# Kernel tuning notes

Measured on AMD Instinct MI355X. Metric: run time of the kernel, lower is better.

The kernel has to match this reference:

```python
import jax, jax.numpy as jnp
import numpy as np

D = 512
B = 8
N = 4096  # h = w = 64 grid


def _rmsnorm(x, eps=1e-6):
    # SimpleRMSNorm (no learned scale)
    return x * jax.lax.rsqrt(jnp.mean(jnp.square(x), axis=-1, keepdims=True) + eps)


def setup_inputs() -> dict:
    key = jax.random.key(0)
    ks = jax.random.split(key, 8)
    s = 1.0 / np.sqrt(D)
    return {
        "x": jax.random.normal(ks[0], (B, N, D), jnp.float32),
        "lower_bound": jax.random.uniform(ks[1], (1,), jnp.float32),
        "W_in": jax.random.normal(ks[2], (D, D), jnp.float32) * s,
        "b_in": jnp.zeros((D,), jnp.float32),
        "W_f": jax.random.normal(ks[3], (D, D), jnp.float32) * s,
        "b_f": jnp.zeros((D,), jnp.float32),
        "theta": jax.random.normal(ks[4], (D,), jnp.float32),
        "W_g": jax.random.normal(ks[5], (D, D), jnp.float32) * s,
        "b_g": jnp.zeros((D,), jnp.float32),
        "W_out": jax.random.normal(ks[6], (D, D), jnp.float32) * s,
        "b_out": jnp.zeros((D,), jnp.float32),
    }


def _gated_scan(decay, u, axis, reverse):
    # linear recurrence h_t = decay_t * h_{t-1} + u_t via associative scan
    def comb(e1, e2):
        a1, x1 = e1
        a2, x2 = e2
        return a1 * a2, a2 * x1 + x2
    _, y = jax.lax.associative_scan(comb, (decay, u), axis=axis, reverse=reverse)
    return y


def reference(x, lower_bound, W_in, b_in, W_f, b_f, theta, W_g, b_g, W_out, b_out):
    b, n, d = x.shape
    h = int(np.sqrt(n))
    w = n // h
    # b n d -> n b d -> h w b d
    xg = jnp.transpose(x, (1, 0, 2)).reshape(h, w, b, d)
    u = jax.nn.silu(xg @ W_in + b_in)              # candidate input
    f = jax.nn.sigmoid(xg @ W_f + b_f)             # forget gate
    lam = lower_bound + (1.0 - lower_bound) * f    # lower-bounded decay magnitude
    # complex decay lam * exp(i theta); complex input (1 - lam) * u
    decay = (lam * jnp.cos(theta) + 1j * (lam * jnp.sin(theta))).astype(jnp.complex64)
    inp = ((1.0 - lam) * u).astype(jnp.complex64)
    # bidirectional 2D scan: forward/backward over both grid axes (non-causal)
    hidden = jnp.zeros_like(u)
    for axis in (0, 1):
        for rev in (False, True):
            hidden = hidden + _gated_scan(decay, inp, axis, rev).real
    g = jax.nn.sigmoid(xg @ W_g + b_g)             # output gate
    y = (g * _rmsnorm(hidden)) @ W_out + b_out
    # h w b d -> n b d -> b n d
    return jnp.transpose(y.reshape(n, b, d), (1, 0, 2))
```

## Files before the change

### kernel.cpp

```cpp
#include <hip/hip_runtime.h>
#include <math.h>

#define DD 512
#define HG 64
#define M_ROWS 32768
#define ELEMS ((size_t)M_ROWS * DD)
#define LOG2E 1.44269504088896340736f

typedef __attribute__((ext_vector_type(8))) _Float16 f16x8;
typedef __attribute__((ext_vector_type(2))) _Float16 f16x2;
typedef __attribute__((ext_vector_type(4))) float f32x4;

__device__ __forceinline__ float fexp2_(float x) { return __builtin_amdgcn_exp2f(x); }
__device__ __forceinline__ float frcp_(float x)  { return __builtin_amdgcn_rcpf(x); }
__device__ __forceinline__ float fsig_(float v)  { return frcp_(1.0f + fexp2_(-v * LOG2E)); }

__global__ __launch_bounds__(256) void prep(
    const float* __restrict__ x, _Float16* __restrict__ x16,
    const float* __restrict__ W0, const float* __restrict__ W1,
    const float* __restrict__ W2, const float* __restrict__ W3,
    _Float16* __restrict__ WT)
{
    __shared__ float tile[64][65];
    if (blockIdx.x < 8192) {
        const size_t i = ((size_t)blockIdx.x * 256 + threadIdx.x) * 8;
        const float4 a = *(const float4*)&x[i];
        const float4 b = *(const float4*)&x[i + 4];
        f16x8 h;
        h[0] = (_Float16)a.x; h[1] = (_Float16)a.y;
        h[2] = (_Float16)a.z; h[3] = (_Float16)a.w;
        h[4] = (_Float16)b.x; h[5] = (_Float16)b.y;
        h[6] = (_Float16)b.z; h[7] = (_Float16)b.w;
        *(f16x8*)&x16[i] = h;
        return;
    }
    const int wb = blockIdx.x - 8192;
    const int z = wb >> 6;
    const int rem = wb & 63;
    const int n0 = (rem & 7) * 64, k0 = (rem >> 3) * 64;
    const float* W = (z == 0) ? W0 : (z == 1) ? W1 : (z == 2) ? W2 : W3;
    _Float16* dst = WT + (size_t)z * DD * DD;
    const int t = threadIdx.x;
    const int tr = t >> 6, tc = t & 63;
#pragma unroll
    for (int p = 0; p < 16; ++p)
        tile[p * 4 + tr][tc] = W[(size_t)(k0 + p * 4 + tr) * DD + n0 + tc];
    __syncthreads();
#pragma unroll
    for (int p = 0; p < 16; ++p) {
        const int nn = p * 4 + tr;
        dst[(size_t)(n0 + nn) * DD + k0 + tc] = (_Float16)tile[tc][nn];
    }
}

template <int MODE>
__global__ __launch_bounds__(256) void gemm_f16(
    const _Float16* __restrict__ A, const _Float16* __restrict__ WT,
    const float* __restrict__ b0, const float* __restrict__ b1,
    const float* __restrict__ b2, const float* __restrict__ lb_ptr,
    void* __restrict__ o0, void* __restrict__ o1, void* __restrict__ o2)
{
    __shared__ __align__(16) _Float16 As[2][128][32];
    __shared__ __align__(16) _Float16 Bs[2][128][32];

    const int NB = (MODE == 0) ? 12 : 4;
    const int lin = blockIdx.x;
    const int xcd = lin & 7;
    const int n_idx = (lin >> 3) % NB;
    const int mq = lin / (8 * NB);
    const int m0 = (xcd + 8 * mq) * 128;
    const int n0 = n_idx * 128;

    const int tid  = threadIdx.x;
    const int wave = tid >> 6;
    const int lane = tid & 63;
    const int wm = wave >> 1, wn = wave & 1;
    const int lrow = lane & 15;
    const int lk   = lane >> 4;

    const int srow  = lane >> 2;
    const int skoff = ((lane & 3) ^ ((lane >> 3) & 3)) * 8;
    const int ksw   = (lk ^ ((lrow >> 1) & 3)) * 8;

    f32x4 acc[4][4];
#pragma unroll
    for (int i = 0; i < 4; ++i)
#pragma unroll
        for (int j = 0; j < 4; ++j) acc[i][j] = (f32x4)(0.f);

    for (int k0 = 0; k0 < DD; k0 += 64) {
#pragma unroll
        for (int h = 0; h < 2; ++h) {
#pragma unroll
            for (int i = 0; i < 2; ++i) {
                const int row = wave * 32 + i * 16;
                const _Float16* bsrc =
                    WT + (size_t)(n0 + row + srow) * DD + k0 + h * 32 + skoff;
                __builtin_amdgcn_global_load_lds(
                    (const __attribute__((address_space(1))) void*)bsrc,
                    (__attribute__((address_space(3))) void*)&Bs[h][row][0], 16, 0, 0);
                const _Float16* asrc =
                    A + (size_t)(m0 + row + srow) * DD + k0 + h * 32 + skoff;
                __builtin_amdgcn_global_load_lds(
                    (const __attribute__((address_space(1))) void*)asrc,
                    (__attribute__((address_space(3))) void*)&As[h][row][0], 16, 0, 0);
            }
        }
        __syncthreads();
#pragma unroll
        for (int h = 0; h < 2; ++h) {
            f16x8 afr[4], bfr[4];
#pragma unroll
            for (int t = 0; t < 4; ++t) {
                afr[t] = *(const f16x8*)&As[h][wm * 64 + t * 16 + lrow][ksw];
                bfr[t] = *(const f16x8*)&Bs[h][wn * 64 + t * 16 + lrow][ksw];
            }
#pragma unroll
            for (int mt = 0; mt < 4; ++mt)
#pragma unroll
                for (int nt = 0; nt < 4; ++nt)
                    acc[mt][nt] = __builtin_amdgcn_mfma_f32_16x16x32_f16(
                        afr[mt], bfr[nt], acc[mt][nt], 0, 0, 0);
        }
        __syncthreads();
    }

    if (MODE == 0) {
        const int seg = n_idx >> 2;
        const float lbv = lb_ptr[0];
        const float* bias = (seg == 0) ? b0 : (seg == 1) ? b1 : b2;
        _Float16* outp = (seg == 0) ? (_Float16*)o0
                       : (seg == 1) ? (_Float16*)o1 : (_Float16*)o2;
        const int cb = (n_idx & 3) * 128 + wn * 64;
#pragma unroll
        for (int mt = 0; mt < 4; ++mt) {
#pragma unroll
            for (int nt = 0; nt < 4; ++nt) {
                const int col = cb + nt * 16 + lrow;
                const float bcol = bias[col];
#pragma unroll
                for (int r = 0; r < 4; ++r) {
                    const int row = m0 + wm * 64 + mt * 16 + lk * 4 + r;
                    const float v = acc[mt][nt][r] + bcol;
                    float res;
                    if (seg == 0)      res = (1.0f - lbv) * frcp_(1.0f + fexp2_(v * LOG2E));
                    else if (seg == 1) res = v * fsig_(v);
                    else               res = fsig_(v);
                    outp[(size_t)row * DD + col] = (_Float16)res;
                }
            }
        }
    } else {
        float* outp = (float*)o0;
#pragma unroll
        for (int mt = 0; mt < 4; ++mt) {
#pragma unroll
            for (int nt = 0; nt < 4; ++nt) {
                const int col = n0 + wn * 64 + nt * 16 + lrow;
                const float bcol = b0[col];
#pragma unroll
                for (int r = 0; r < 4; ++r) {
                    const int row = m0 + wm * 64 + mt * 16 + lk * 4 + r;
                    outp[(size_t)row * DD + col] = acc[mt][nt][r] + bcol;
                }
            }
        }
    }
}

#define CH 4
#define CL 16

#define STEP(K, YR0, YI0, YR1, YI1) {                                      \
    const float dm0_ = (float)dmr[K][0], dm1_ = (float)dmr[K][1];          \
    const float lm0_ = 1.0f - dm0_, lm1_ = 1.0f - dm1_;                    \
    float nr_ = fmaf(lm0_, c0 * (YR0) - s0 * (YI0), dm0_ * (float)ur[K][0]); \
    YI0 = lm0_ * (c0 * (YI0) + s0 * (YR0)); YR0 = nr_;                     \
    nr_ = fmaf(lm1_, c1 * (YR1) - s1 * (YI1), dm1_ * (float)ur[K][1]);     \
    YI1 = lm1_ * (c1 * (YI1) + s1 * (YR1)); YR1 = nr_; }

__global__ __launch_bounds__(256, 4) void scan2(
    const _Float16* __restrict__ dm, const _Float16* __restrict__ u,
    const float* __restrict__ theta,
    _Float16* __restrict__ ha, _Float16* __restrict__ hb)
{
    __shared__ float ex[CH][64][13];

    const int blk  = blockIdx.x & 2047;
    const bool is_i = blockIdx.x >= 2048;
    const int tid   = threadIdx.x;
    const int chunk = tid >> 6;
    const int dpl   = tid & 63;
    const int dpg   = blk & 3;
    const int line  = blk >> 2;
    const int d0    = (dpg * 64 + dpl) * 2;

    size_t base, stride;
    _Float16* hout;
    if (!is_i) {
        base = (size_t)line * (HG * DD) + d0; stride = DD; hout = ha;
    } else {
        const int bb = line >> 6, j = line & 63;
        base = (size_t)bb * (HG * HG * DD) + (size_t)j * DD + d0;
        stride = (size_t)HG * DD; hout = hb;
    }
    const size_t cbase = base + (size_t)(chunk * CL) * stride;

    float s0, c0, s1, c1;
    sincosf(theta[d0], &s0, &c0);
    sincosf(theta[d0 + 1], &s1, &c1);

    f16x2 dmr[CL], ur[CL];
#pragma unroll
    for (int k = 0; k < CL; ++k) {
        dmr[k] = *(const f16x2*)&dm[cbase + (size_t)k * stride];
        ur[k]  = *(const f16x2*)&u [cbase + (size_t)k * stride];
    }

    float fr0 = 0.f, fi0 = 0.f, fr1 = 0.f, fi1 = 0.f;
    float P0 = 1.f, P1 = 1.f;
#pragma unroll
    for (int k = 0; k < CL; ++k) {
        const float dm0_ = (float)dmr[k][0], dm1_ = (float)dmr[k][1];
        const float lm0_ = 1.0f - dm0_, lm1_ = 1.0f - dm1_;
        P0 *= lm0_; P1 *= lm1_;
        float nr_ = fmaf(lm0_, c0 * fr0 - s0 * fi0, dm0_ * (float)ur[k][0]);
        fi0 = lm0_ * (c0 * fi0 + s0 * fr0); fr0 = nr_;
        nr_ = fmaf(lm1_, c1 * fr1 - s1 * fi1, dm1_ * (float)ur[k][1]);
        fi1 = lm1_ * (c1 * fi1 + s1 * fr1); fr1 = nr_;
    }
    float br0 = 0.f, bi0 = 0.f, br1 = 0.f, bi1 = 0.f;
#pragma unroll
    for (int k = CL - 1; k >= 0; --k) STEP(k, br0, bi0, br1, bi1);

    float rc0 = c0, rs0 = s0, rc1 = c1, rs1 = s1;
#pragma unroll
    for (int q = 0; q < 4; ++q) {
        float t0 = rc0 * rc0 - rs0 * rs0; rs0 = 2.f * rc0 * rs0; rc0 = t0;
        float t1 = rc1 * rc1 - rs1 * rs1; rs1 = 2.f * rc1 * rs1; rc1 = t1;
    }

    {
        float* e = ex[chunk][dpl];
        e[0]  = P0 * rc0; e[1]  = P0 * rs0;
        e[2]  = fr0;      e[3]  = fi0;
        e[4]  = br0;      e[5]  = bi0;
        e[6]  = P1 * rc1; e[7]  = P1 * rs1;
        e[8]  = fr1;      e[9]  = fi1;
        e[10] = br1;      e[11] = bi1;
    }
    __syncthreads();

    float cfr0 = 0.f, cfi0 = 0.f, cfr1 = 0.f, cfi1 = 0.f;
    for (int cc = 0; cc < chunk; ++cc) {
        const float* e = ex[cc][dpl];
        float nr = e[2] + e[0] * cfr0 - e[1] * cfi0;
        cfi0     = e[3] + e[0] * cfi0 + e[1] * cfr0;
        cfr0 = nr;
        nr       = e[8] + e[6] * cfr1 - e[7] * cfi1;
        cfi1     = e[9] + e[6] * cfi1 + e[7] * cfr1;
        cfr1 = nr;
    }
    float cbr0 = 0.f, cbi0 = 0.f, cbr1 = 0.f, cbi1 = 0.f;
    for (int cc = CH - 1; cc > chunk; --cc) {
        const float* e = ex[cc][dpl];
        float nr = e[4] + e[0] * cbr0 - e[1] * cbi0;
        cbi0     = e[5] + e[0] * cbi0 + e[1] * cbr0;
        cbr0 = nr;
        nr       = e[10] + e[6] * cbr1 - e[7] * cbi1;
        cbi1     = e[11] + e[6] * cbi1 + e[7] * cbr1;
        cbr1 = nr;
    }

    float yr0 = cfr0, yi0 = cfi0, yr1 = cfr1, yi1 = cfi1;
    f16x2 fres[CL];
#pragma unroll
    for (int k = 0; k < CL; ++k) {
        STEP(k, yr0, yi0, yr1, yi1);
        f16x2 p; p[0] = (_Float16)yr0; p[1] = (_Float16)yr1;
        fres[k] = p;
    }
    yr0 = cbr0; yi0 = cbi0; yr1 = cbr1; yi1 = cbi1;
#pragma unroll
    for (int k = CL - 1; k >= 0; --k) {
        STEP(k, yr0, yi0, yr1, yi1);
        f16x2 o;
        o[0] = (_Float16)((float)fres[k][0] + yr0);
        o[1] = (_Float16)((float)fres[k][1] + yr1);
        *(f16x2*)&hout[cbase + (size_t)k * stride] = o;
    }
}
#undef STEP

__global__ __launch_bounds__(256) void gate_rmsnorm(
    const _Float16* __restrict__ ha, const _Float16* __restrict__ hb,
    const _Float16* __restrict__ g, _Float16* __restrict__ v)
{
    const int row = blockIdx.x;
    const int t = threadIdx.x;
    const size_t b0 = (size_t)row * DD + t * 2;
    const f16x2 a = *(const f16x2*)&ha[b0];
    const f16x2 b = *(const f16x2*)&hb[b0];
    const float h0 = (float)a[0] + (float)b[0];
    const float h1 = (float)a[1] + (float)b[1];
    float ss = h0 * h0 + h1 * h1;
#pragma unroll
    for (int off = 32; off > 0; off >>= 1) ss += __shfl_down(ss, off, 64);
    __shared__ float wsum[4];
    __shared__ float rms_s;
    if ((t & 63) == 0) wsum[t >> 6] = ss;
    __syncthreads();
    if (t == 0) {
        const float tot = wsum[0] + wsum[1] + wsum[2] + wsum[3];
        rms_s = rsqrtf(tot * (1.0f / (float)DD) + 1e-6f);
    }
    __syncthreads();
    const float rms = rms_s;
    const f16x2 gg = *(const f16x2*)&g[b0];
    f16x2 o;
    o[0] = (_Float16)((float)gg[0] * h0 * rms);
    o[1] = (_Float16)((float)gg[1] * h1 * rms);
    *(f16x2*)&v[b0] = o;
}

extern "C" void kernel_launch(void* const* d_in, const int* in_sizes, int n_in,
                              void* d_out, int out_size, void* d_ws, size_t ws_size,
                              hipStream_t stream)
{
    const float* x     = (const float*)d_in[0];
    const float* lb    = (const float*)d_in[1];
    const float* W_in  = (const float*)d_in[2];
    const float* b_in  = (const float*)d_in[3];
    const float* W_f   = (const float*)d_in[4];
    const float* b_f   = (const float*)d_in[5];
    const float* theta = (const float*)d_in[6];
    const float* W_g   = (const float*)d_in[7];
    const float* b_g   = (const float*)d_in[8];
    const float* W_out = (const float*)d_in[9];
    const float* b_out = (const float*)d_in[10];

    float* out = (float*)d_out;
    char* wsb  = (char*)d_ws;

    _Float16* dm_v = (_Float16*)wsb;
    _Float16* u_b  = (_Float16*)(wsb + ELEMS * 2);
    _Float16* g_b  = (_Float16*)(wsb + ELEMS * 4);
    _Float16* WT   = (_Float16*)(wsb + ELEMS * 6);
    const size_t WSEG = (size_t)DD * DD;

    _Float16* ha  = (_Float16*)d_out;
    _Float16* x16 = (_Float16*)((char*)d_out + ELEMS * 2);
    _Float16* hb  = x16;

    prep<<<8448, 256, 0, stream>>>(x, x16, W_f, W_in, W_g, W_out, WT);

    gemm_f16<0><<<3072, 256, 0, stream>>>(x16, WT, b_f, b_in, b_g, lb,
                                          dm_v, u_b, g_b);

    scan2<<<4096, 256, 0, stream>>>(dm_v, u_b, theta, ha, hb);

    gate_rmsnorm<<<M_ROWS, 256, 0, stream>>>(ha, hb, g_b, dm_v);

    gemm_f16<1><<<1024, 256, 0, stream>>>(dm_v, WT + 3 * WSEG, b_out, nullptr,
                                          nullptr, nullptr, out, nullptr, nullptr);
}
```

Before: 292.8 us.

## Triple-buffer GEMM K-loop with async LDS loads and single barrier per step

Replaces the double-sync, load-then-compute K loop of the f16 MFMA GEMM with a 3-stage ring buffer in shared memory. Global-to-LDS loads are issued two 32-wide K slices ahead, and a partial vmcnt wait plus one barrier per step lets loads overlap the MFMA work. It also raises wave priority around the MFMA block with s_setprio. The cost is more LDS per block, which can lower occupancy, and correctness depends on the hand-written vmcnt counts.

Result: no change. 295.9 us (+1.0%).

```diff
diff --git a/kernel.cpp b/kernel.cpp
--- a/kernel.cpp
+++ b/kernel.cpp
@@ -60,8 +60,8 @@
     const float* __restrict__ b2, const float* __restrict__ lb_ptr,
     void* __restrict__ o0, void* __restrict__ o1, void* __restrict__ o2)
 {
-    __shared__ __align__(16) _Float16 As[2][128][32];
-    __shared__ __align__(16) _Float16 Bs[2][128][32];
+    __shared__ __align__(16) _Float16 As[3][128][32];
+    __shared__ __align__(16) _Float16 Bs[3][128][32];
 
     const int NB = (MODE == 0) ? 12 : 4;
     const int lin = blockIdx.x;
@@ -82,48 +82,64 @@
     const int skoff = ((lane & 3) ^ ((lane >> 3) & 3)) * 8;
     const int ksw   = (lk ^ ((lrow >> 1) & 3)) * 8;
 
+    const _Float16* a_base = A  + (size_t)(m0 + srow) * DD + skoff;
+    const _Float16* b_base = WT + (size_t)(n0 + srow) * DD + skoff;
+
     f32x4 acc[4][4];
 #pragma unroll
     for (int i = 0; i < 4; ++i)
 #pragma unroll
         for (int j = 0; j < 4; ++j) acc[i][j] = (f32x4)(0.f);
 
-    for (int k0 = 0; k0 < DD; k0 += 64) {
-#pragma unroll
-        for (int h = 0; h < 2; ++h) {
-#pragma unroll
-            for (int i = 0; i < 2; ++i) {
-                const int row = wave * 32 + i * 16;
-                const _Float16* bsrc =
-                    WT + (size_t)(n0 + row + srow) * DD + k0 + h * 32 + skoff;
-                __builtin_amdgcn_global_load_lds(
-                    (const __attribute__((address_space(1))) void*)bsrc,
-                    (__attribute__((address_space(3))) void*)&Bs[h][row][0], 16, 0, 0);
-                const _Float16* asrc =
-                    A + (size_t)(m0 + row + srow) * DD + k0 + h * 32 + skoff;
-                __builtin_amdgcn_global_load_lds(
-                    (const __attribute__((address_space(1))) void*)asrc,
-                    (__attribute__((address_space(3))) void*)&As[h][row][0], 16, 0, 0);
-            }
+#define STAGE(S, KK) do {                                                     \
+    _Pragma("unroll")                                                         \
+    for (int i_ = 0; i_ < 2; ++i_) {                                          \
+        const int row_ = wave * 32 + i_ * 16;                                 \
+        __builtin_amdgcn_global_load_lds(                                     \
+            (const __attribute__((address_space(1))) void*)                   \
+                (b_base + (size_t)row_ * DD + (KK)),                          \
+            (__attribute__((address_space(3))) void*)&Bs[S][row_][0], 16, 0, 0); \
+        __builtin_amdgcn_global_load_lds(                                     \
+            (const __attribute__((address_space(1))) void*)                   \
+                (a_base + (size_t)row_ * DD + (KK)),                          \
+            (__attribute__((address_space(3))) void*)&As[S][row_][0], 16, 0, 0); \
+    } } while (0)
+
+#define COMPUTE(S) do {                                                       \
+    f16x8 afr[4], bfr[4];                                                     \
+    _Pragma("unroll")                                                         \
+    for (int q_ = 0; q_ < 4; ++q_) {                                          \
+        afr[q_] = *(const f16x8*)&As[S][wm * 64 + q_ * 16 + lrow][ksw];       \
+        bfr[q_] = *(const f16x8*)&Bs[S][wn * 64 + q_ * 16 + lrow][ksw];       \
+    }                                                                         \
+    __builtin_amdgcn_s_setprio(1);                                            \
+    _Pragma("unroll")                                                         \
+    for (int mt_ = 0; mt_ < 4; ++mt_)                                         \
+        _Pragma("unroll")                                                     \
+        for (int nt_ = 0; nt_ < 4; ++nt_)                                     \
+            acc[mt_][nt_] = __builtin_amdgcn_mfma_f32_16x16x32_f16(           \
+                afr[mt_], bfr[nt_], acc[mt_][nt_], 0, 0, 0);                  \
+    __builtin_amdgcn_s_setprio(0);                                            \
+    } while (0)
+
+    STAGE(0, 0);
+    STAGE(1, 32);
+    int rs = 0, ws = 2;
+    for (int t = 0; t < 15; ++t) {
+        asm volatile("s_waitcnt vmcnt(4)" ::: "memory");
+        __builtin_amdgcn_s_barrier();
+        if (t < 14) {
+            STAGE(ws, (t + 2) * 32);
+            ws = (ws == 2) ? 0 : ws + 1;
         }
-        __syncthreads();
-#pragma unroll
-        for (int h = 0; h < 2; ++h) {
-            f16x8 afr[4], bfr[4];
-#pragma unroll
-            for (int t = 0; t < 4; ++t) {
-                afr[t] = *(const f16x8*)&As[h][wm * 64 + t * 16 + lrow][ksw];
-                bfr[t] = *(const f16x8*)&Bs[h][wn * 64 + t * 16 + lrow][ksw];
-            }
-#pragma unroll
-            for (int mt = 0; mt < 4; ++mt)
-#pragma unroll
-                for (int nt = 0; nt < 4; ++nt)
-                    acc[mt][nt] = __builtin_amdgcn_mfma_f32_16x16x32_f16(
-                        afr[mt], bfr[nt], acc[mt][nt], 0, 0, 0);
-        }
-        __syncthreads();
-    }
+        COMPUTE(rs);
+        rs = (rs == 2) ? 0 : rs + 1;
+    }
+    asm volatile("s_waitcnt vmcnt(0)" ::: "memory");
+    __builtin_amdgcn_s_barrier();
+    COMPUTE(rs);
+#undef STAGE
+#undef COMPUTE
 
     if (MODE == 0) {
         const int seg = n_idx >> 2;
```

## Rewrite GEMMs as 256x256-tile 8-wave kernel with interleaved async LDS prefetch

Applied to the files above, without the earlier changes.

Replaces the 128x128 double-buffered GEMM with a 256x256 tile, 512-thread kernel that runs over 64-wide K-steps. It interleaves global_load_lds prefetches of the next stages with MFMA quarters, using explicit vmcnt waits, barriers and setprio. It also applies an XOR swizzle on 128-byte LDS rows. The aim is higher arithmetic intensity and overlap of loads with MFMA work, at the cost of 128 KB of LDS per block, many more accumulator registers, and fewer blocks (768 and 256) that may underfill the GPU's CUs.

Result: faster. 283.0 us (-3.4%).

```diff
diff --git a/kernel.cpp b/kernel.cpp
--- a/kernel.cpp
+++ b/kernel.cpp
@@ -54,115 +54,188 @@
 }
 
 template <int MODE>
-__global__ __launch_bounds__(256) void gemm_f16(
+__global__ __launch_bounds__(512, 2) void gemm8p(
     const _Float16* __restrict__ A, const _Float16* __restrict__ WT,
     const float* __restrict__ b0, const float* __restrict__ b1,
     const float* __restrict__ b2, const float* __restrict__ lb_ptr,
     void* __restrict__ o0, void* __restrict__ o1, void* __restrict__ o2)
 {
-    __shared__ __align__(16) _Float16 As[2][128][32];
-    __shared__ __align__(16) _Float16 Bs[2][128][32];
-
-    const int NB = (MODE == 0) ? 12 : 4;
+    __shared__ __align__(16) _Float16 As[2][256][64];
+    __shared__ __align__(16) _Float16 Bs[2][256][64];
+
+    const int NB = (MODE == 0) ? 6 : 2;
     const int lin = blockIdx.x;
     const int xcd = lin & 7;
-    const int n_idx = (lin >> 3) % NB;
-    const int mq = lin / (8 * NB);
-    const int m0 = (xcd + 8 * mq) * 128;
-    const int n0 = n_idx * 128;
+    const int qq  = lin >> 3;
+    const int n_idx = qq % NB;
+    const int mq  = qq / NB;
+    const int m0 = (xcd + 8 * mq) * 256;
+    const int n0 = n_idx * 256;
 
     const int tid  = threadIdx.x;
-    const int wave = tid >> 6;
+    const int wv   = tid >> 6;
     const int lane = tid & 63;
-    const int wm = wave >> 1, wn = wave & 1;
+    const int wm = wv >> 2, wn = wv & 3;
     const int lrow = lane & 15;
     const int lk   = lane >> 4;
 
-    const int srow  = lane >> 2;
-    const int skoff = ((lane & 3) ^ ((lane >> 3) & 3)) * 8;
-    const int ksw   = (lk ^ ((lrow >> 1) & 3)) * 8;
-
-    f32x4 acc[4][4];
-#pragma unroll
-    for (int i = 0; i < 4; ++i)
+    const int srow8 = wv * 8 + (lane >> 3);
+    const int sswz  = ((lane & 7) ^ (lane >> 3)) * 8;
+
+    const _Float16* Ag = A  + (size_t)m0 * DD;
+    const _Float16* Bg = WT + (size_t)n0 * DD;
+
+    f32x4 acc[8][4];
+#pragma unroll
+    for (int i = 0; i < 8; ++i)
 #pragma unroll
         for (int j = 0; j < 4; ++j) acc[i][j] = (f32x4)(0.f);
 
-    for (int k0 = 0; k0 < DD; k0 += 64) {
-#pragma unroll
-        for (int h = 0; h < 2; ++h) {
-#pragma unroll
-            for (int i = 0; i < 2; ++i) {
-                const int row = wave * 32 + i * 16;
-                const _Float16* bsrc =
-                    WT + (size_t)(n0 + row + srow) * DD + k0 + h * 32 + skoff;
-                __builtin_amdgcn_global_load_lds(
-                    (const __attribute__((address_space(1))) void*)bsrc,
-                    (__attribute__((address_space(3))) void*)&Bs[h][row][0], 16, 0, 0);
-                const _Float16* asrc =
-                    A + (size_t)(m0 + row + srow) * DD + k0 + h * 32 + skoff;
-                __builtin_amdgcn_global_load_lds(
-                    (const __attribute__((address_space(1))) void*)asrc,
-                    (__attribute__((address_space(3))) void*)&As[h][row][0], 16, 0, 0);
-            }
-        }
-        __syncthreads();
-#pragma unroll
-        for (int h = 0; h < 2; ++h) {
-            f16x8 afr[4], bfr[4];
-#pragma unroll
-            for (int t = 0; t < 4; ++t) {
-                afr[t] = *(const f16x8*)&As[h][wm * 64 + t * 16 + lrow][ksw];
-                bfr[t] = *(const f16x8*)&Bs[h][wn * 64 + t * 16 + lrow][ksw];
-            }
-#pragma unroll
-            for (int mt = 0; mt < 4; ++mt)
-#pragma unroll
-                for (int nt = 0; nt < 4; ++nt)
-                    acc[mt][nt] = __builtin_amdgcn_mfma_f32_16x16x32_f16(
-                        afr[mt], bfr[nt], acc[mt][nt], 0, 0, 0);
-        }
-        __syncthreads();
-    }
+#define STG(LDSBUF, GPTR, P_, HALF_, KT_) do {                                 \
+    _Pragma("unroll")                                                          \
+    for (int j_ = 0; j_ < 2; ++j_) {                                           \
+        __builtin_amdgcn_global_load_lds(                                      \
+            (const __attribute__((address_space(1))) void*)                    \
+              (GPTR + (size_t)((HALF_)*128 + j_*64 + srow8) * DD               \
+                     + (KT_)*64 + sswz),                                       \
+            (__attribute__((address_space(3))) void*)                          \
+              &LDSBUF[P_][(HALF_)*128 + j_*64 + wv*8][0], 16, 0, 0);           \
+    } } while (0)
+
+#define LDA(P_, HA_) do {                                                      \
+    _Pragma("unroll")                                                          \
+    for (int q_ = 0; q_ < 4; ++q_)                                             \
+    _Pragma("unroll")                                                          \
+    for (int ks_ = 0; ks_ < 2; ++ks_)                                          \
+        aA[q_][ks_] = *(const f16x8*)((const char*)&As[P_][0][0]               \
+            + (size_t)((wm*64 + q_*16 + (HA_)*128 + lrow) * 128                \
+            + (((ks_*4 + lk) ^ (lrow & 7)) * 16)));                            \
+    } while (0)
+
+#define LDB(DST_, P_, HB_) do {                                                \
+    _Pragma("unroll")                                                          \
+    for (int q_ = 0; q_ < 2; ++q_)                                             \
+    _Pragma("unroll")                                                          \
+    for (int ks_ = 0; ks_ < 2; ++ks_)                                          \
+        DST_[q_][ks_] = *(const f16x8*)((const char*)&Bs[P_][0][0]             \
+            + (size_t)((wn*32 + q_*16 + (HB_)*128 + lrow) * 128                \
+            + (((ks_*4 + lk) ^ (lrow & 7)) * 16)));                            \
+    } while (0)
+
+#define MMQ(HA_, BSET_, BOFF_) do {                                            \
+    __builtin_amdgcn_s_setprio(1);                                             \
+    _Pragma("unroll")                                                          \
+    for (int q_ = 0; q_ < 4; ++q_)                                             \
+    _Pragma("unroll")                                                          \
+    for (int n_ = 0; n_ < 2; ++n_)                                             \
+    _Pragma("unroll")                                                          \
+    for (int ks_ = 0; ks_ < 2; ++ks_)                                          \
+        acc[(HA_)*4 + q_][(BOFF_) + n_] =                                      \
+            __builtin_amdgcn_mfma_f32_16x16x32_f16(                            \
+                aA[q_][ks_], BSET_[n_][ks_], acc[(HA_)*4 + q_][(BOFF_) + n_],  \
+                0, 0, 0);                                                      \
+    __builtin_amdgcn_s_setprio(0);                                             \
+    } while (0)
+
+#define BAR __builtin_amdgcn_s_barrier()
+#define VM(N_) asm volatile("s_waitcnt vmcnt(" #N_ ")" ::: "memory")
+
+    f16x8 aA[4][2], bB0[2][2], bB1[2][2];
+
+    STG(As, Ag, 0, 0, 0);
+    STG(Bs, Bg, 0, 0, 0);
+    STG(Bs, Bg, 0, 1, 0);
+    STG(As, Ag, 0, 1, 0);
+    STG(As, Ag, 1, 0, 1);
+    STG(Bs, Bg, 1, 0, 1);
+    STG(Bs, Bg, 1, 1, 1);
+    VM(10); BAR;
+
+    for (int g = 0; g < 6; ++g) {
+        const int p = g & 1;
+        LDA(p, 0); LDB(bB0, p, 0);
+        STG(As, Ag, p ^ 1, 1, g + 1);
+        BAR;
+        MMQ(0, bB0, 0);
+        VM(10); BAR;
+        LDB(bB1, p, 1);
+        STG(As, Ag, p, 0, g + 2);
+        BAR;
+        MMQ(0, bB1, 2);
+        VM(10); BAR;
+        LDA(p, 1);
+        STG(Bs, Bg, p, 0, g + 2);
+        BAR;
+        MMQ(1, bB1, 2);
+        BAR;
+        STG(Bs, Bg, p, 1, g + 2);
+        BAR;
+        MMQ(1, bB0, 0);
+        VM(10); BAR;
+    }
+
+    LDA(0, 0); LDB(bB0, 0, 0);
+    STG(As, Ag, 1, 1, 7);
+    BAR; MMQ(0, bB0, 0); VM(10); BAR;
+    LDB(bB1, 0, 1);
+    BAR; MMQ(0, bB1, 2); VM(8); BAR;
+    LDA(0, 1);
+    BAR; MMQ(1, bB1, 2); BAR;
+    MMQ(1, bB0, 0);
+    VM(4); BAR;
+
+    LDA(1, 0); LDB(bB0, 1, 0);
+    BAR; MMQ(0, bB0, 0); VM(2); BAR;
+    LDB(bB1, 1, 1);
+    BAR; MMQ(0, bB1, 2); VM(0); BAR;
+    LDA(1, 1);
+    BAR; MMQ(1, bB1, 2); BAR;
+    MMQ(1, bB0, 0);
+
+#undef STG
+#undef LDA
+#undef LDB
+#undef MMQ
+#undef BAR
+#undef VM
 
     if (MODE == 0) {
-        const int seg = n_idx >> 2;
+        const int seg = n_idx >> 1;
         const float lbv = lb_ptr[0];
         const float* bias = (seg == 0) ? b0 : (seg == 1) ? b1 : b2;
         _Float16* outp = (seg == 0) ? (_Float16*)o0
                        : (seg == 1) ? (_Float16*)o1 : (_Float16*)o2;
-        const int cb = (n_idx & 3) * 128 + wn * 64;
-#pragma unroll
-        for (int mt = 0; mt < 4; ++mt) {
-#pragma unroll
-            for (int nt = 0; nt < 4; ++nt) {
-                const int col = cb + nt * 16 + lrow;
+        const int cbase = (n_idx & 1) * 256 + wn * 32;
+#pragma unroll
+        for (int a = 0; a < 8; ++a) {
+            const int row = m0 + wm * 64 + (a & 3) * 16 + (a >> 2) * 128 + lk * 4;
+#pragma unroll
+            for (int b = 0; b < 4; ++b) {
+                const int col = cbase + (b & 1) * 16 + (b >> 1) * 128 + lrow;
                 const float bcol = bias[col];
 #pragma unroll
                 for (int r = 0; r < 4; ++r) {
-                    const int row = m0 + wm * 64 + mt * 16 + lk * 4 + r;
-                    const float v = acc[mt][nt][r] + bcol;
+                    const float v = acc[a][b][r] + bcol;
                     float res;
                     if (seg == 0)      res = (1.0f - lbv) * frcp_(1.0f + fexp2_(v * LOG2E));
                     else if (seg == 1) res = v * fsig_(v);
                     else               res = fsig_(v);
-                    outp[(size_t)row * DD + col] = (_Float16)res;
+                    outp[(size_t)(row + r) * DD + col] = (_Float16)res;
                 }
             }
         }
     } else {
         float* outp = (float*)o0;
 #pragma unroll
-        for (int mt = 0; mt < 4; ++mt) {
-#pragma unroll
-            for (int nt = 0; nt < 4; ++nt) {
-                const int col = n0 + wn * 64 + nt * 16 + lrow;
+        for (int a = 0; a < 8; ++a) {
+            const int row = m0 + wm * 64 + (a & 3) * 16 + (a >> 2) * 128 + lk * 4;
+#pragma unroll
+            for (int b = 0; b < 4; ++b) {
+                const int col = n0 + wn * 32 + (b & 1) * 16 + (b >> 1) * 128 + lrow;
                 const float bcol = b0[col];
 #pragma unroll
-                for (int r = 0; r < 4; ++r) {
-                    const int row = m0 + wm * 64 + mt * 16 + lk * 4 + r;
-                    outp[(size_t)row * DD + col] = acc[mt][nt][r] + bcol;
-                }
+                for (int r = 0; r < 4; ++r)
+                    outp[(size_t)(row + r) * DD + col] = acc[a][b][r] + bcol;
             }
         }
     }
@@ -354,13 +427,13 @@
 
     prep<<<8448, 256, 0, stream>>>(x, x16, W_f, W_in, W_g, W_out, WT);
 
-    gemm_f16<0><<<3072, 256, 0, stream>>>(x16, WT, b_f, b_in, b_g, lb,
-                                          dm_v, u_b, g_b);
+    gemm8p<0><<<768, 512, 0, stream>>>(x16, WT, b_f, b_in, b_g, lb,
+                                       dm_v, u_b, g_b);
 
     scan2<<<4096, 256, 0, stream>>>(dm_v, u_b, theta, ha, hb);
 
     gate_rmsnorm<<<M_ROWS, 256, 0, stream>>>(ha, hb, g_b, dm_v);
 
-    gemm_f16<1><<<1024, 256, 0, stream>>>(dm_v, WT + 3 * WSEG, b_out, nullptr,
-                                          nullptr, nullptr, out, nullptr, nullptr);
+    gemm8p<1><<<256, 512, 0, stream>>>(dm_v, WT + 3 * WSEG, b_out, nullptr,
+                                       nullptr, nullptr, out, nullptr, nullptr);
 }
```
